# Kernel optimization log

Hardware: AMD Instinct MI355X
Metric: run time of the kernel (lower is better)

The kernel has to match this reference:

```python
import jax, jax.numpy as jnp
import numpy as np

N_NODES = 50000
N_EDGES = 800000
IN_CH = 128
HID = 64
OUT_CH = 10
N_GRAPHS = 512


def setup_inputs() -> dict:
    key = jax.random.key(0)
    ks = jax.random.split(key, 16)
    x = jax.random.normal(ks[0], (N_NODES, IN_CH), dtype=jnp.float32)
    edge_index = jax.random.randint(ks[1], (2, N_EDGES), 0, N_NODES, dtype=jnp.int64)
    batch = jnp.sort(jax.random.randint(ks[2], (N_NODES,), 0, N_GRAPHS, dtype=jnp.int64))
    def lin(k, fan_in, fan_out):
        bound = 1.0 / np.sqrt(fan_in)
        kw, kb = jax.random.split(k)
        w = jax.random.uniform(kw, (fan_in, fan_out), minval=-bound, maxval=bound, dtype=jnp.float32)
        b = jax.random.uniform(kb, (fan_out,), minval=-bound, maxval=bound, dtype=jnp.float32)
        return w, b
    w0a, b0a = lin(ks[3], IN_CH, HID)
    w0b, b0b = lin(ks[4], HID, HID)
    w1a, b1a = lin(ks[5], HID, HID)
    w1b, b1b = lin(ks[6], HID, HID)
    fcw, fcb = lin(ks[7], HID, OUT_CH)
    eps0 = jnp.zeros((), dtype=jnp.float32)  # train_eps=True, init 0
    eps1 = jnp.zeros((), dtype=jnp.float32)
    return {"x": x, "edge_index": edge_index, "batch": batch,
            "eps0": eps0, "w0a": w0a, "b0a": b0a, "w0b": w0b, "b0b": b0b,
            "eps1": eps1, "w1a": w1a, "b1a": b1a, "w1b": w1b, "b1b": b1b,
            "fcw": fcw, "fcb": fcb}


def _gin_layer(x, src, dst, eps, wa, ba, wb, bb):
    # sum-aggregate neighbor messages: agg[i] = sum_{(j->i) in E} x[j]
    agg = jax.ops.segment_sum(x[src], dst, num_segments=N_NODES)
    h = (1.0 + eps) * x + agg
    h = jax.nn.relu(h @ wa + ba)
    h = jax.nn.relu(h @ wb + bb)  # MLP ends in ReLU; outer F.relu is a no-op
    return h


def reference(x, edge_index, batch, eps0, w0a, b0a, w0b, b0b,
              eps1, w1a, b1a, w1b, b1b, fcw, fcb):
    src, dst = edge_index[0], edge_index[1]
    h = _gin_layer(x, src, dst, eps0, w0a, b0a, w0b, b0b)
    # dropout skipped (inference)
    h = _gin_layer(h, src, dst, eps1, w1a, b1a, w1b, b1b)
    pooled = jax.ops.segment_sum(h, batch, num_segments=N_GRAPHS)  # [G, HID]
    logits = pooled @ fcw + fcb
    return jax.nn.log_softmax(logits, axis=1)
```

## Files before the change

### kernel.cpp

```cpp
#include <hip/hip_runtime.h>
#include <math.h>

#define IN_CH 128
#define HID 64
#define OUT_CH 10

typedef unsigned int uint32;
typedef unsigned char u8;
typedef unsigned short bf16u;
typedef __attribute__((ext_vector_type(8))) short bf16x8;
typedef __attribute__((ext_vector_type(4))) float f32x4;
typedef __attribute__((ext_vector_type(2))) float f32x2;

static __device__ inline bf16u f2bf(float f) {
    uint32 u = __float_as_uint(f);
    u += 0x7fff + ((u >> 16) & 1);
    return (bf16u)(u >> 16);
}
static __device__ inline uint32 pack2(float a, float b) {
    return (uint32)f2bf(a) | ((uint32)f2bf(b) << 16);
}
static __device__ inline u8 f2fp8(float v) {
    uint32 p = __builtin_amdgcn_cvt_pk_fp8_f32(v, v, 0, false);
    return (u8)(p & 0xff);
}
static __device__ inline void acc_fp8x4(uint32 u, float& a0, float& a1,
                                        float& a2, float& a3) {
    f32x2 lo = __builtin_amdgcn_cvt_pk_f32_fp8((int)u, false);
    f32x2 hi = __builtin_amdgcn_cvt_pk_f32_fp8((int)u, true);
    a0 += lo.x; a1 += lo.y; a2 += hi.x; a3 += hi.y;
}

static __device__ inline void gather_nbrs8(
    const uint32* __restrict__ y8, const int* __restrict__ col,
    int rs, int re, int h, int c2,
    float& a0, float& a1, float& a2, float& a3)
{
    int j = rs;
    for (; j + 16 <= re; j += 16) {
        int s0 = col[j + h];
        int s1 = col[j + 4 + h];
        int s2 = col[j + 8 + h];
        int s3 = col[j + 12 + h];
        uint32 u0 = y8[(long)s0 * 16 + c2];
        uint32 u1 = y8[(long)s1 * 16 + c2];
        uint32 u2 = y8[(long)s2 * 16 + c2];
        uint32 u3 = y8[(long)s3 * 16 + c2];
        acc_fp8x4(u0, a0, a1, a2, a3);
        acc_fp8x4(u1, a0, a1, a2, a3);
        acc_fp8x4(u2, a0, a1, a2, a3);
        acc_fp8x4(u3, a0, a1, a2, a3);
    }
    for (; j + 4 <= re; j += 4) {
        uint32 u = y8[(long)col[j + h] * 16 + c2];
        acc_fp8x4(u, a0, a1, a2, a3);
    }
    int r = re - j;
    if (h < r) {
        uint32 u = y8[(long)col[j + h] * 16 + c2];
        acc_fp8x4(u, a0, a1, a2, a3);
    }
}

__global__ __launch_bounds__(256) void k_count(
    const int* __restrict__ dst, int* __restrict__ cnt,
    int* __restrict__ pos, int E)
{
    int e = blockIdx.x * 256 + threadIdx.x;
    if (e < E) pos[e] = atomicAdd(&cnt[dst[e]], 1);
}

__global__ __launch_bounds__(256) void k_scan(
    const int* __restrict__ cnt, int* __restrict__ row_ptr,
    int* __restrict__ partials, int* __restrict__ counter, int N, int E, int nch)
{
    __shared__ int red[256];
    int tid = threadIdx.x;
    int bid = blockIdx.x;
    long base = (long)bid * 1024 + tid * 4;
    int v[4]; int s = 0;
    #pragma unroll
    for (int i = 0; i < 4; i++) {
        long idx = base + i;
        v[i] = (idx < N) ? cnt[idx] : 0;
        s += v[i];
    }
    red[tid] = s;
    __syncthreads();
    for (int off = 1; off < 256; off <<= 1) {
        int t = (tid >= off) ? red[tid - off] : 0;
        __syncthreads();
        red[tid] += t;
        __syncthreads();
    }
    int myexcl = red[tid] - s;
    if (tid == 255) {
        __hip_atomic_store(&partials[bid], red[255], __ATOMIC_RELEASE,
                           __HIP_MEMORY_SCOPE_AGENT);
        atomicAdd(counter, 1);
    }
    if (tid == 0) {
        while (__hip_atomic_load(counter, __ATOMIC_ACQUIRE,
                                 __HIP_MEMORY_SCOPE_AGENT) < nch) { }
    }
    __syncthreads();
    int off = 0;
    for (int i = tid; i < bid; i += 256)
        off += __hip_atomic_load(&partials[i], __ATOMIC_RELAXED,
                                 __HIP_MEMORY_SCOPE_AGENT);
    __syncthreads();
    red[tid] = off;
    __syncthreads();
    for (int o = 128; o; o >>= 1) {
        if (tid < o) red[tid] += red[tid + o];
        __syncthreads();
    }
    int run = red[0] + myexcl;
    #pragma unroll
    for (int i = 0; i < 4; i++) {
        long idx = base + i;
        if (idx < N) row_ptr[idx] = run;
        run += v[i];
    }
    if (bid == 0 && tid == 0) row_ptr[N] = E;
}

__global__ __launch_bounds__(256) void k_place(
    const int* __restrict__ src, const int* __restrict__ dst,
    const int* __restrict__ row_ptr, const int* __restrict__ pos,
    int* __restrict__ col, int E)
{
    int e = blockIdx.x * 256 + threadIdx.x;
    if (e >= E) return;
    col[row_ptr[dst[e]] + pos[e]] = src[e];
}

__global__ __launch_bounds__(256, 6) void k_lin0(
    const float4* __restrict__ x4, const float* __restrict__ w,
    u8* __restrict__ y, int N)
{
    __shared__ __align__(16) uint32 t32[16 * 68];
    int tid = threadIdx.x;
    int wid = tid >> 6, lane = tid & 63;
    int quad = lane >> 4, n15 = lane & 15;
    int mycol = wid * 16 + n15;
    bf16x8 fb[4];
    #pragma unroll
    for (int s = 0; s < 4; s++)
        #pragma unroll
        for (int j = 0; j < 8; j++)
            fb[s][j] = (short)f2bf(w[(s * 32 + quad * 8 + j) * HID + mycol]);
    int snode = tid >> 4, sk = tid & 15;
    for (long g0 = (long)blockIdx.x * 16; g0 < N; g0 += (long)gridDim.x * 16) {
        long node = g0 + snode;
        if (node < N) {
            float4 v0 = x4[node * 32 + sk * 2];
            float4 v1 = x4[node * 32 + sk * 2 + 1];
            uint32 p[4] = {pack2(v0.x, v0.y), pack2(v0.z, v0.w),
                           pack2(v1.x, v1.y), pack2(v1.z, v1.w)};
            *(uint4*)((char*)t32 + snode * 272 + sk * 16) = *(uint4*)p;
        }
        __syncthreads();
        f32x4 acc = {0.f, 0.f, 0.f, 0.f};
        #pragma unroll
        for (int s = 0; s < 4; s++) {
            bf16x8 a = *(const bf16x8*)((const char*)t32 + n15 * 272 + s * 64 + quad * 16);
            acc = __builtin_amdgcn_mfma_f32_16x16x32_bf16(a, fb[s], acc, 0, 0, 0);
        }
        #pragma unroll
        for (int r = 0; r < 4; r++) {
            long n = g0 + quad * 4 + r;
            if (n < N) y[n * HID + mycol] = f2fp8(acc[r]);
        }
        __syncthreads();
    }
}

__global__ __launch_bounds__(256, 6) void k_agg0f(
    const uint32* __restrict__ y8, const int* __restrict__ row_ptr,
    const int* __restrict__ col, const float* __restrict__ epsp,
    const float* __restrict__ ba, const float* __restrict__ wb,
    const float* __restrict__ bb, const float* __restrict__ w1a,
    u8* __restrict__ y1, int N)
{
    __shared__ __align__(16) uint32 t32[16 * 36];
    __shared__ __align__(16) uint32 h32[16 * 36];
    int tid = threadIdx.x;
    int wid = tid >> 6, lane = tid & 63;
    int c2 = lane & 15, h = lane >> 4;
    int quad = lane >> 4, n15 = lane & 15;
    int n0 = wid * 4;
    int mycol = wid * 16 + n15;
    float e = 1.f + epsp[0];
    float4 bav = ((const float4*)ba)[c2];
    float bbv = bb[mycol];
    bf16x8 fb[2], f1[2];
    #pragma unroll
    for (int s = 0; s < 2; s++)
        #pragma unroll
        for (int j = 0; j < 8; j++) {
            fb[s][j] = (short)f2bf(wb[(s * 32 + quad * 8 + j) * HID + mycol]);
            f1[s][j] = (short)f2bf(w1a[(s * 32 + quad * 8 + j) * HID + mycol]);
        }
    for (long g0 = (long)blockIdx.x * 16; g0 < N; g0 += (long)gridDim.x * 16) {
        for (int m = 0; m < 4; m++) {
            long node = g0 + n0 + m;
            float a0 = 0.f, a1 = 0.f, a2 = 0.f, a3 = 0.f;
            if (node < N) {
                int rs = row_ptr[node], re = row_ptr[node + 1];
                gather_nbrs8(y8, col, rs, re, h, c2, a0, a1, a2, a3);
                if (h == 0) {
                    f32x2 lo = __builtin_amdgcn_cvt_pk_f32_fp8((int)y8[node * 16 + c2], false);
                    f32x2 hi = __builtin_amdgcn_cvt_pk_f32_fp8((int)y8[node * 16 + c2], true);
                    a0 = fmaf(e, lo.x, a0); a1 = fmaf(e, lo.y, a1);
                    a2 = fmaf(e, hi.x, a2); a3 = fmaf(e, hi.y, a3);
                }
            }
            a0 += __shfl_xor(a0, 16); a0 += __shfl_xor(a0, 32);
            a1 += __shfl_xor(a1, 16); a1 += __shfl_xor(a1, 32);
            a2 += __shfl_xor(a2, 16); a2 += __shfl_xor(a2, 32);
            a3 += __shfl_xor(a3, 16); a3 += __shfl_xor(a3, 32);
            if (h == 0) {
                t32[(n0 + m) * 36 + 2 * c2]     = pack2(fmaxf(a0 + bav.x, 0.f),
                                                        fmaxf(a1 + bav.y, 0.f));
                t32[(n0 + m) * 36 + 2 * c2 + 1] = pack2(fmaxf(a2 + bav.z, 0.f),
                                                        fmaxf(a3 + bav.w, 0.f));
            }
        }
        __syncthreads();
        f32x4 acc = {bbv, bbv, bbv, bbv};
        {
            bf16x8 a0 = *(const bf16x8*)((const char*)t32 + n15 * 144 + quad * 16);
            bf16x8 a1 = *(const bf16x8*)((const char*)t32 + n15 * 144 + 64 + quad * 16);
            acc = __builtin_amdgcn_mfma_f32_16x16x32_bf16(a0, fb[0], acc, 0, 0, 0);
            acc = __builtin_amdgcn_mfma_f32_16x16x32_bf16(a1, fb[1], acc, 0, 0, 0);
        }
        #pragma unroll
        for (int r = 0; r < 4; r++)
            ((short*)h32)[(quad * 4 + r) * 72 + mycol] = (short)f2bf(fmaxf(acc[r], 0.f));
        __syncthreads();
        f32x4 acc2 = {0.f, 0.f, 0.f, 0.f};
        {
            bf16x8 a0 = *(const bf16x8*)((const char*)h32 + n15 * 144 + quad * 16);
            bf16x8 a1 = *(const bf16x8*)((const char*)h32 + n15 * 144 + 64 + quad * 16);
            acc2 = __builtin_amdgcn_mfma_f32_16x16x32_bf16(a0, f1[0], acc2, 0, 0, 0);
            acc2 = __builtin_amdgcn_mfma_f32_16x16x32_bf16(a1, f1[1], acc2, 0, 0, 0);
        }
        #pragma unroll
        for (int r = 0; r < 4; r++) {
            long n = g0 + quad * 4 + r;
            if (n < N) y1[n * HID + mycol] = f2fp8(acc2[r]);
        }
    }
}

__global__ __launch_bounds__(256, 6) void k_agg1(
    const uint32* __restrict__ y8, const int* __restrict__ row_ptr,
    const int* __restrict__ col, const float* __restrict__ epsp,
    const float* __restrict__ ba, const float* __restrict__ wb,
    const float* __restrict__ bb, const int* __restrict__ batch,
    float* __restrict__ pooled, int N)
{
    __shared__ __align__(16) uint32 t32[16 * 36];
    int tid = threadIdx.x;
    int wid = tid >> 6, lane = tid & 63;
    int c2 = lane & 15, h = lane >> 4;
    int quad = lane >> 4, n15 = lane & 15;
    int n0 = wid * 4;
    int mycol = wid * 16 + n15;
    float e = 1.f + epsp[0];
    float4 bav = ((const float4*)ba)[c2];
    float bbv = bb[mycol];
    bf16x8 fb[2];
    #pragma unroll
    for (int s = 0; s < 2; s++)
        #pragma unroll
        for (int j = 0; j < 8; j++)
            fb[s][j] = (short)f2bf(wb[(s * 32 + quad * 8 + j) * HID + mycol]);
    for (long g0 = (long)blockIdx.x * 16; g0 < N; g0 += (long)gridDim.x * 16) {
        for (int m = 0; m < 4; m++) {
            long node = g0 + n0 + m;
            float a0 = 0.f, a1 = 0.f, a2 = 0.f, a3 = 0.f;
            if (node < N) {
                int rs = row_ptr[node], re = row_ptr[node + 1];
                gather_nbrs8(y8, col, rs, re, h, c2, a0, a1, a2, a3);
                if (h == 0) {
                    f32x2 lo = __builtin_amdgcn_cvt_pk_f32_fp8((int)y8[node * 16 + c2], false);
                    f32x2 hi = __builtin_amdgcn_cvt_pk_f32_fp8((int)y8[node * 16 + c2], true);
                    a0 = fmaf(e, lo.x, a0); a1 = fmaf(e, lo.y, a1);
                    a2 = fmaf(e, hi.x, a2); a3 = fmaf(e, hi.y, a3);
                }
            }
            a0 += __shfl_xor(a0, 16); a0 += __shfl_xor(a0, 32);
            a1 += __shfl_xor(a1, 16); a1 += __shfl_xor(a1, 32);
            a2 += __shfl_xor(a2, 16); a2 += __shfl_xor(a2, 32);
            a3 += __shfl_xor(a3, 16); a3 += __shfl_xor(a3, 32);
            if (h == 0) {
                t32[(n0 + m) * 36 + 2 * c2]     = pack2(fmaxf(a0 + bav.x, 0.f),
                                                        fmaxf(a1 + bav.y, 0.f));
                t32[(n0 + m) * 36 + 2 * c2 + 1] = pack2(fmaxf(a2 + bav.z, 0.f),
                                                        fmaxf(a3 + bav.w, 0.f));
            }
        }
        __syncthreads();
        f32x4 acc = {bbv, bbv, bbv, bbv};
        {
            bf16x8 a0 = *(const bf16x8*)((const char*)t32 + n15 * 144 + quad * 16);
            bf16x8 a1 = *(const bf16x8*)((const char*)t32 + n15 * 144 + 64 + quad * 16);
            acc = __builtin_amdgcn_mfma_f32_16x16x32_bf16(a0, fb[0], acc, 0, 0, 0);
            acc = __builtin_amdgcn_mfma_f32_16x16x32_bf16(a1, fb[1], acc, 0, 0, 0);
        }
        float rv[4];
        #pragma unroll
        for (int r = 0; r < 4; r++) rv[r] = fmaxf(acc[r], 0.f);
        int nv = (int)((N - g0) < 16 ? (N - g0) : 16);
        int bf_ = batch[g0], bl_ = batch[g0 + nv - 1];
        if (bf_ == bl_) {
            float s = 0.f;
            #pragma unroll
            for (int r = 0; r < 4; r++)
                if (quad * 4 + r < nv) s += rv[r];
            s += __shfl_xor(s, 16);
            s += __shfl_xor(s, 32);
            if (quad == 0)
                atomicAdd(&pooled[(long)bf_ * HID + mycol], s);
        } else {
            #pragma unroll
            for (int r = 0; r < 4; r++) {
                long n = g0 + quad * 4 + r;
                if (n < N)
                    atomicAdd(&pooled[(long)batch[n] * HID + mycol], rv[r]);
            }
        }
        __syncthreads();
    }
}

__global__ __launch_bounds__(64) void k_head(
    const float* __restrict__ pooled, const float* __restrict__ fcw,
    const float* __restrict__ fcb, float* __restrict__ out)
{
    int g = blockIdx.x;
    int l = threadIdx.x;
    float logit = -INFINITY;
    if (l < OUT_CH) {
        float acc = fcb[l];
        #pragma unroll
        for (int k = 0; k < HID; k++)
            acc = fmaf(pooled[g * HID + k], fcw[k * OUT_CH + l], acc);
        logit = acc;
    }
    float m = logit;
    #pragma unroll
    for (int off = 32; off; off >>= 1) m = fmaxf(m, __shfl_xor(m, off));
    float ex = (l < OUT_CH) ? expf(logit - m) : 0.0f;
    float s = ex;
    #pragma unroll
    for (int off = 32; off; off >>= 1) s += __shfl_xor(s, off);
    if (l < OUT_CH) out[g * OUT_CH + l] = logit - m - logf(s);
}

extern "C" void kernel_launch(void* const* d_in, const int* in_sizes, int n_in,
                              void* d_out, int out_size, void* d_ws, size_t ws_size,
                              hipStream_t stream) {
    const float* x    = (const float*)d_in[0];
    const int*   ei   = (const int*)d_in[1];
    const int*   batch= (const int*)d_in[2];
    const float* eps0 = (const float*)d_in[3];
    const float* w0a  = (const float*)d_in[4];
    const float* b0a  = (const float*)d_in[5];
    const float* w0b  = (const float*)d_in[6];
    const float* b0b  = (const float*)d_in[7];
    const float* eps1 = (const float*)d_in[8];
    const float* w1a  = (const float*)d_in[9];
    const float* b1a  = (const float*)d_in[10];
    const float* w1b  = (const float*)d_in[11];
    const float* b1b  = (const float*)d_in[12];
    const float* fcw  = (const float*)d_in[13];
    const float* fcb  = (const float*)d_in[14];
    float* out = (float*)d_out;

    const int N = in_sizes[0] / IN_CH;
    const int E = in_sizes[1] / 2;
    const int G = out_size / OUT_CH;
    const int* src = ei;
    const int* dst = ei + E;

    char* ws = (char*)d_ws;
    int*    row_ptr  = (int*)(ws);
    int*    colv     = (int*)(ws + 200064);
    u8*     y0       = (u8*)(ws + 3400064);
    u8*     y1       = (u8*)(ws + 6600064);
    int*    cnt      = (int*)(ws + 9800064);
    int*    counter  = (int*)(ws + 10000064);
    int*    partials = (int*)(ws + 10000128);
    float*  pooled   = (float*)(ws + 10000384);
    int*    pos      = (int*)(ws + 10131456);

    hipMemsetAsync(cnt, 0, 331392, stream);

    int eb = (E + 255) / 256;
    int nb = (N + 31) / 32;
    int nch = (N + 1023) / 1024;
    k_count<<<eb, 256, 0, stream>>>(dst, cnt, pos, E);
    k_scan<<<nch, 256, 0, stream>>>(cnt, row_ptr, partials, counter, N, E, nch);
    k_place<<<eb, 256, 0, stream>>>(src, dst, row_ptr, pos, colv, E);

    k_lin0<<<nb, 256, 0, stream>>>((const float4*)x, w0a, y0, N);
    k_agg0f<<<nb, 256, 0, stream>>>((const uint32*)y0, row_ptr, colv, eps0,
                                    b0a, w0b, b0b, w1a, y1, N);
    k_agg1<<<nb, 256, 0, stream>>>((const uint32*)y1, row_ptr, colv, eps1,
                                   b1a, w1b, b1b, batch, pooled, N);
    k_head<<<G, 64, 0, stream>>>(pooled, fcw, fcb, out);
}
```

Before: 218.0 us.

## Fuse degree count into lin0, place edges via atomic cursors, one node per lane group

Folds the edge degree-counting atomics into the first linear kernel and drops the per-edge position array, so edges are placed through atomic write cursors that the scan initialises. The aggregation kernels now give each 16-lane group its own node instead of splitting one node's neighbours across four groups. That removes the cross-group shuffle reductions and the serial loop over four nodes. In exchange, CSR column order within a node becomes nondeterministic, and high-degree nodes now fall on a single lane group, which adds load imbalance within each wave.

```diff
diff --git a/kernel.cpp b/kernel.cpp
--- a/kernel.cpp
+++ b/kernel.cpp
@@ -31,114 +31,41 @@
     a0 += lo.x; a1 += lo.y; a2 += hi.x; a3 += hi.y;
 }
 
-static __device__ inline void gather_nbrs8(
+static __device__ inline void gather_group(
     const uint32* __restrict__ y8, const int* __restrict__ col,
-    int rs, int re, int h, int c2,
+    int rs, int re, int c2,
     float& a0, float& a1, float& a2, float& a3)
 {
     int j = rs;
-    for (; j + 16 <= re; j += 16) {
-        int s0 = col[j + h];
-        int s1 = col[j + 4 + h];
-        int s2 = col[j + 8 + h];
-        int s3 = col[j + 12 + h];
-        uint32 u0 = y8[(long)s0 * 16 + c2];
-        uint32 u1 = y8[(long)s1 * 16 + c2];
-        uint32 u2 = y8[(long)s2 * 16 + c2];
-        uint32 u3 = y8[(long)s3 * 16 + c2];
+    for (; j + 4 <= re; j += 4) {
+        int s0 = col[j];
+        int s1 = col[j + 1];
+        int s2 = col[j + 2];
+        int s3 = col[j + 3];
+        uint32 u0 = y8[s0 * 16 + c2];
+        uint32 u1 = y8[s1 * 16 + c2];
+        uint32 u2 = y8[s2 * 16 + c2];
+        uint32 u3 = y8[s3 * 16 + c2];
         acc_fp8x4(u0, a0, a1, a2, a3);
         acc_fp8x4(u1, a0, a1, a2, a3);
         acc_fp8x4(u2, a0, a1, a2, a3);
         acc_fp8x4(u3, a0, a1, a2, a3);
     }
-    for (; j + 4 <= re; j += 4) {
-        uint32 u = y8[(long)col[j + h] * 16 + c2];
+    for (; j < re; ++j) {
+        uint32 u = y8[col[j] * 16 + c2];
         acc_fp8x4(u, a0, a1, a2, a3);
     }
-    int r = re - j;
-    if (h < r) {
-        uint32 u = y8[(long)col[j + h] * 16 + c2];
-        acc_fp8x4(u, a0, a1, a2, a3);
-    }
-}
-
-__global__ __launch_bounds__(256) void k_count(
+}
+
+__global__ __launch_bounds__(256, 6) void k_pre(
     const int* __restrict__ dst, int* __restrict__ cnt,
-    int* __restrict__ pos, int E)
-{
-    int e = blockIdx.x * 256 + threadIdx.x;
-    if (e < E) pos[e] = atomicAdd(&cnt[dst[e]], 1);
-}
-
-__global__ __launch_bounds__(256) void k_scan(
-    const int* __restrict__ cnt, int* __restrict__ row_ptr,
-    int* __restrict__ partials, int* __restrict__ counter, int N, int E, int nch)
-{
-    __shared__ int red[256];
-    int tid = threadIdx.x;
-    int bid = blockIdx.x;
-    long base = (long)bid * 1024 + tid * 4;
-    int v[4]; int s = 0;
-    #pragma unroll
-    for (int i = 0; i < 4; i++) {
-        long idx = base + i;
-        v[i] = (idx < N) ? cnt[idx] : 0;
-        s += v[i];
-    }
-    red[tid] = s;
-    __syncthreads();
-    for (int off = 1; off < 256; off <<= 1) {
-        int t = (tid >= off) ? red[tid - off] : 0;
-        __syncthreads();
-        red[tid] += t;
-        __syncthreads();
-    }
-    int myexcl = red[tid] - s;
-    if (tid == 255) {
-        __hip_atomic_store(&partials[bid], red[255], __ATOMIC_RELEASE,
-                           __HIP_MEMORY_SCOPE_AGENT);
-        atomicAdd(counter, 1);
-    }
-    if (tid == 0) {
-        while (__hip_atomic_load(counter, __ATOMIC_ACQUIRE,
-                                 __HIP_MEMORY_SCOPE_AGENT) < nch) { }
-    }
-    __syncthreads();
-    int off = 0;
-    for (int i = tid; i < bid; i += 256)
-        off += __hip_atomic_load(&partials[i], __ATOMIC_RELAXED,
-                                 __HIP_MEMORY_SCOPE_AGENT);
-    __syncthreads();
-    red[tid] = off;
-    __syncthreads();
-    for (int o = 128; o; o >>= 1) {
-        if (tid < o) red[tid] += red[tid + o];
-        __syncthreads();
-    }
-    int run = red[0] + myexcl;
-    #pragma unroll
-    for (int i = 0; i < 4; i++) {
-        long idx = base + i;
-        if (idx < N) row_ptr[idx] = run;
-        run += v[i];
-    }
-    if (bid == 0 && tid == 0) row_ptr[N] = E;
-}
-
-__global__ __launch_bounds__(256) void k_place(
-    const int* __restrict__ src, const int* __restrict__ dst,
-    const int* __restrict__ row_ptr, const int* __restrict__ pos,
-    int* __restrict__ col, int E)
-{
-    int e = blockIdx.x * 256 + threadIdx.x;
-    if (e >= E) return;
-    col[row_ptr[dst[e]] + pos[e]] = src[e];
-}
-
-__global__ __launch_bounds__(256, 6) void k_lin0(
     const float4* __restrict__ x4, const float* __restrict__ w,
-    u8* __restrict__ y, int N)
-{
+    u8* __restrict__ y, int N, int E)
+{
+    int gt = blockIdx.x * 256 + threadIdx.x;
+    for (int e = gt; e < E; e += gridDim.x * 256)
+        atomicAdd(&cnt[dst[e]], 1);
+
     __shared__ __align__(16) uint32 t32[16 * 68];
     int tid = threadIdx.x;
     int wid = tid >> 6, lane = tid & 63;
@@ -174,6 +101,71 @@
         }
         __syncthreads();
     }
+}
+
+__global__ __launch_bounds__(256) void k_scan(
+    const int* __restrict__ cnt, int* __restrict__ row_ptr,
+    int* __restrict__ wptr, int* __restrict__ partials,
+    int* __restrict__ counter, int N, int E, int nch)
+{
+    __shared__ int red[256];
+    int tid = threadIdx.x;
+    int bid = blockIdx.x;
+    long base = (long)bid * 1024 + tid * 4;
+    int v[4]; int s = 0;
+    #pragma unroll
+    for (int i = 0; i < 4; i++) {
+        long idx = base + i;
+        v[i] = (idx < N) ? cnt[idx] : 0;
+        s += v[i];
+    }
+    red[tid] = s;
+    __syncthreads();
+    for (int off = 1; off < 256; off <<= 1) {
+        int t = (tid >= off) ? red[tid - off] : 0;
+        __syncthreads();
+        red[tid] += t;
+        __syncthreads();
+    }
+    int myexcl = red[tid] - s;
+    if (tid == 255) {
+        __hip_atomic_store(&partials[bid], red[255], __ATOMIC_RELEASE,
+                           __HIP_MEMORY_SCOPE_AGENT);
+        atomicAdd(counter, 1);
+    }
+    if (tid == 0) {
+        while (__hip_atomic_load(counter, __ATOMIC_ACQUIRE,
+                                 __HIP_MEMORY_SCOPE_AGENT) < nch) { }
+    }
+    __syncthreads();
+    int off = 0;
+    for (int i = tid; i < bid; i += 256)
+        off += __hip_atomic_load(&partials[i], __ATOMIC_RELAXED,
+                                 __HIP_MEMORY_SCOPE_AGENT);
+    __syncthreads();
+    red[tid] = off;
+    __syncthreads();
+    for (int o = 128; o; o >>= 1) {
+        if (tid < o) red[tid] += red[tid + o];
+        __syncthreads();
+    }
+    int run = red[0] + myexcl;
+    #pragma unroll
+    for (int i = 0; i < 4; i++) {
+        long idx = base + i;
+        if (idx < N) { row_ptr[idx] = run; wptr[idx] = run; }
+        run += v[i];
+    }
+    if (bid == 0 && tid == 0) row_ptr[N] = E;
+}
+
+__global__ __launch_bounds__(256) void k_place(
+    const int* __restrict__ src, const int* __restrict__ dst,
+    int* __restrict__ wptr, int* __restrict__ col, int E)
+{
+    int e = blockIdx.x * 256 + threadIdx.x;
+    if (e >= E) return;
+    col[atomicAdd(&wptr[dst[e]], 1)] = src[e];
 }
 
 __global__ __launch_bounds__(256, 6) void k_agg0f(
@@ -203,29 +195,20 @@
             f1[s][j] = (short)f2bf(w1a[(s * 32 + quad * 8 + j) * HID + mycol]);
         }
     for (long g0 = (long)blockIdx.x * 16; g0 < N; g0 += (long)gridDim.x * 16) {
-        for (int m = 0; m < 4; m++) {
-            long node = g0 + n0 + m;
+        long node = g0 + n0 + h;
+        if (node < N) {
+            int rs = row_ptr[node], re = row_ptr[node + 1];
+            uint32 us = y8[node * 16 + c2];
             float a0 = 0.f, a1 = 0.f, a2 = 0.f, a3 = 0.f;
-            if (node < N) {
-                int rs = row_ptr[node], re = row_ptr[node + 1];
-                gather_nbrs8(y8, col, rs, re, h, c2, a0, a1, a2, a3);
-                if (h == 0) {
-                    f32x2 lo = __builtin_amdgcn_cvt_pk_f32_fp8((int)y8[node * 16 + c2], false);
-                    f32x2 hi = __builtin_amdgcn_cvt_pk_f32_fp8((int)y8[node * 16 + c2], true);
-                    a0 = fmaf(e, lo.x, a0); a1 = fmaf(e, lo.y, a1);
-                    a2 = fmaf(e, hi.x, a2); a3 = fmaf(e, hi.y, a3);
-                }
-            }
-            a0 += __shfl_xor(a0, 16); a0 += __shfl_xor(a0, 32);
-            a1 += __shfl_xor(a1, 16); a1 += __shfl_xor(a1, 32);
-            a2 += __shfl_xor(a2, 16); a2 += __shfl_xor(a2, 32);
-            a3 += __shfl_xor(a3, 16); a3 += __shfl_xor(a3, 32);
-            if (h == 0) {
-                t32[(n0 + m) * 36 + 2 * c2]     = pack2(fmaxf(a0 + bav.x, 0.f),
-                                                        fmaxf(a1 + bav.y, 0.f));
-                t32[(n0 + m) * 36 + 2 * c2 + 1] = pack2(fmaxf(a2 + bav.z, 0.f),
-                                                        fmaxf(a3 + bav.w, 0.f));
-            }
+            gather_group(y8, col, rs, re, c2, a0, a1, a2, a3);
+            f32x2 lo = __builtin_amdgcn_cvt_pk_f32_fp8((int)us, false);
+            f32x2 hi = __builtin_amdgcn_cvt_pk_f32_fp8((int)us, true);
+            a0 = fmaf(e, lo.x, a0); a1 = fmaf(e, lo.y, a1);
+            a2 = fmaf(e, hi.x, a2); a3 = fmaf(e, hi.y, a3);
+            t32[(n0 + h) * 36 + 2 * c2]     = pack2(fmaxf(a0 + bav.x, 0.f),
+                                                    fmaxf(a1 + bav.y, 0.f));
+            t32[(n0 + h) * 36 + 2 * c2 + 1] = pack2(fmaxf(a2 + bav.z, 0.f),
+                                                    fmaxf(a3 + bav.w, 0.f));
         }
         __syncthreads();
         f32x4 acc = {bbv, bbv, bbv, bbv};
@@ -278,29 +261,20 @@
         for (int j = 0; j < 8; j++)
             fb[s][j] = (short)f2bf(wb[(s * 32 + quad * 8 + j) * HID + mycol]);
     for (long g0 = (long)blockIdx.x * 16; g0 < N; g0 += (long)gridDim.x * 16) {
-        for (int m = 0; m < 4; m++) {
-            long node = g0 + n0 + m;
+        long node = g0 + n0 + h;
+        if (node < N) {
+            int rs = row_ptr[node], re = row_ptr[node + 1];
+            uint32 us = y8[node * 16 + c2];
             float a0 = 0.f, a1 = 0.f, a2 = 0.f, a3 = 0.f;
-            if (node < N) {
-                int rs = row_ptr[node], re = row_ptr[node + 1];
-                gather_nbrs8(y8, col, rs, re, h, c2, a0, a1, a2, a3);
-                if (h == 0) {
-                    f32x2 lo = __builtin_amdgcn_cvt_pk_f32_fp8((int)y8[node * 16 + c2], false);
-                    f32x2 hi = __builtin_amdgcn_cvt_pk_f32_fp8((int)y8[node * 16 + c2], true);
-                    a0 = fmaf(e, lo.x, a0); a1 = fmaf(e, lo.y, a1);
-                    a2 = fmaf(e, hi.x, a2); a3 = fmaf(e, hi.y, a3);
-                }
-            }
-            a0 += __shfl_xor(a0, 16); a0 += __shfl_xor(a0, 32);
-            a1 += __shfl_xor(a1, 16); a1 += __shfl_xor(a1, 32);
-            a2 += __shfl_xor(a2, 16); a2 += __shfl_xor(a2, 32);
-            a3 += __shfl_xor(a3, 16); a3 += __shfl_xor(a3, 32);
-            if (h == 0) {
-                t32[(n0 + m) * 36 + 2 * c2]     = pack2(fmaxf(a0 + bav.x, 0.f),
-                                                        fmaxf(a1 + bav.y, 0.f));
-                t32[(n0 + m) * 36 + 2 * c2 + 1] = pack2(fmaxf(a2 + bav.z, 0.f),
-                                                        fmaxf(a3 + bav.w, 0.f));
-            }
+            gather_group(y8, col, rs, re, c2, a0, a1, a2, a3);
+            f32x2 lo = __builtin_amdgcn_cvt_pk_f32_fp8((int)us, false);
+            f32x2 hi = __builtin_amdgcn_cvt_pk_f32_fp8((int)us, true);
+            a0 = fmaf(e, lo.x, a0); a1 = fmaf(e, lo.y, a1);
+            a2 = fmaf(e, hi.x, a2); a3 = fmaf(e, hi.y, a3);
+            t32[(n0 + h) * 36 + 2 * c2]     = pack2(fmaxf(a0 + bav.x, 0.f),
+                                                    fmaxf(a1 + bav.y, 0.f));
+            t32[(n0 + h) * 36 + 2 * c2 + 1] = pack2(fmaxf(a2 + bav.z, 0.f),
+                                                    fmaxf(a3 + bav.w, 0.f));
         }
         __syncthreads();
         f32x4 acc = {bbv, bbv, bbv, bbv};
@@ -395,18 +369,17 @@
     int*    counter  = (int*)(ws + 10000064);
     int*    partials = (int*)(ws + 10000128);
     float*  pooled   = (float*)(ws + 10000384);
-    int*    pos      = (int*)(ws + 10131456);
+    int*    wptr     = (int*)(ws + 10131456);
 
     hipMemsetAsync(cnt, 0, 331392, stream);
 
     int eb = (E + 255) / 256;
     int nb = (N + 31) / 32;
     int nch = (N + 1023) / 1024;
-    k_count<<<eb, 256, 0, stream>>>(dst, cnt, pos, E);
-    k_scan<<<nch, 256, 0, stream>>>(cnt, row_ptr, partials, counter, N, E, nch);
-    k_place<<<eb, 256, 0, stream>>>(src, dst, row_ptr, pos, colv, E);
-
-    k_lin0<<<nb, 256, 0, stream>>>((const float4*)x, w0a, y0, N);
+    k_pre<<<nb, 256, 0, stream>>>(dst, cnt, (const float4*)x, w0a, y0, N, E);
+    k_scan<<<nch, 256, 0, stream>>>(cnt, row_ptr, wptr, partials, counter, N, E, nch);
+    k_place<<<eb, 256, 0, stream>>>(src, dst, wptr, colv, E);
+
     k_agg0f<<<nb, 256, 0, stream>>>((const uint32*)y0, row_ptr, colv, eps0,
                                     b0a, w0b, b0b, w1a, y1, N);
     k_agg1<<<nb, 256, 0, stream>>>((const uint32*)y1, row_ptr, colv, eps1,
```

New measurement: 227.1 us. +4.2%, slower.
